# Kernel optimization log

Hardware: AMD Instinct MI355X
Metric: run time of the kernel (lower is better)

Reference implementation:

```python
import jax, jax.numpy as jnp
import numpy as np

B, NV, NC, D, E = 16, 8192, 4096, 128, 49152


def _gru_cell(x, h, w_ih, w_hh, b_ih, b_hh):
    """torch.nn.GRUCell math; gate order r, z, n; weights are (3D, D)."""
    gi = x @ w_ih.T + b_ih
    gh = h @ w_hh.T + b_hh
    ir, iz, inn = jnp.split(gi, 3, axis=-1)
    hr, hz, hn = jnp.split(gh, 3, axis=-1)
    r = jax.nn.sigmoid(ir + hr)
    z = jax.nn.sigmoid(iz + hz)
    n = jnp.tanh(inn + r * hn)
    return (1.0 - z) * n + z * h


def _msg_net(x, w1, b1, w2, b2):
    # Linear -> exact GELU -> Linear (torch nn.GELU default is erf-based)
    return jax.nn.gelu(x @ w1.T + b1, approximate=False) @ w2.T + b2


def _spmm(feats, src_idx, dst_idx, n_out):
    """Binary sparse-matrix @ dense: gather rows at src_idx, segment-sum to dst_idx.
    feats: (B, N_src, D) -> (B, n_out, D). Equivalent to torch.sparse.mm(H, feats[i])."""
    gathered = feats[:, src_idx, :]  # (B, E, D)
    return jax.vmap(lambda g: jax.ops.segment_sum(g, dst_idx, num_segments=n_out))(gathered)


def setup_inputs() -> dict:
    key = jax.random.key(0)
    ks = jax.random.split(key, 20)
    s = 0.05
    inp = {
        "v_feats": jax.random.normal(ks[0], (B, NV, D), jnp.float32),
        "c_feats": jax.random.normal(ks[1], (B, NC, D), jnp.float32),
        "edge_chk": jax.random.randint(ks[2], (E,), 0, NC, jnp.int32),
        "edge_var": jax.random.randint(ks[3], (E,), 0, NV, jnp.int32),
        # msg_net: Linear(D,D) -> GELU -> Linear(D,D)
        "msg_w1": jax.random.normal(ks[4], (D, D), jnp.float32) * s,
        "msg_b1": jnp.zeros((D,), jnp.float32),
        "msg_w2": jax.random.normal(ks[5], (D, D), jnp.float32) * s,
        "msg_b2": jnp.zeros((D,), jnp.float32),
        # var_update GRUCell(D, D)
        "var_w_ih": jax.random.normal(ks[6], (3 * D, D), jnp.float32) * s,
        "var_w_hh": jax.random.normal(ks[7], (3 * D, D), jnp.float32) * s,
        "var_b_ih": jnp.zeros((3 * D,), jnp.float32),
        "var_b_hh": jnp.zeros((3 * D,), jnp.float32),
        # chk_update GRUCell(D, D)
        "chk_w_ih": jax.random.normal(ks[8], (3 * D, D), jnp.float32) * s,
        "chk_w_hh": jax.random.normal(ks[9], (3 * D, D), jnp.float32) * s,
        "chk_b_ih": jnp.zeros((3 * D,), jnp.float32),
        "chk_b_hh": jnp.zeros((3 * D,), jnp.float32),
    }
    return inp


def reference(v_feats, c_feats, edge_chk, edge_var,
              msg_w1, msg_b1, msg_w2, msg_b2,
              var_w_ih, var_w_hh, var_b_ih, var_b_hh,
              chk_w_ih, chk_w_hh, chk_b_ih, chk_b_hh):
    b, nv, d = v_feats.shape
    nc = c_feats.shape[1]
    # variable -> check: H @ v_feats (H is binary, rows=checks, cols=vars)
    v_to_c = _spmm(v_feats, edge_var, edge_chk, nc)        # (B, NC, D)
    v_to_c = _msg_net(v_to_c, msg_w1, msg_b1, msg_w2, msg_b2)
    c_new = _gru_cell(v_to_c.reshape(-1, d), c_feats.reshape(-1, d),
                      chk_w_ih, chk_w_hh, chk_b_ih, chk_b_hh).reshape(b, nc, d)
    # check -> variable: H^T @ c_new
    c_to_v = _spmm(c_new, edge_chk, edge_var, nv)          # (B, NV, D)
    c_to_v = _msg_net(c_to_v, msg_w1, msg_b1, msg_w2, msg_b2)
    v_new = _gru_cell(c_to_v.reshape(-1, d), v_feats.reshape(-1, d),
                      var_w_ih, var_w_hh, var_b_ih, var_b_hh).reshape(b, nv, d)
    return (v_new, c_new)
```

## Files before the change

### kernel.cpp

```cpp
#include <hip/hip_runtime.h>

using u16 = unsigned short;
using u32 = unsigned int;
using u64 = unsigned long long;
typedef short short8 __attribute__((ext_vector_type(8)));
typedef unsigned short ushort8 __attribute__((ext_vector_type(8)));
typedef float f32x4 __attribute__((ext_vector_type(4)));

#define GB  16
#define GNV 8192
#define GNC 4096
#define GD  128
#define GE  49152

#define MFMA __builtin_amdgcn_mfma_f32_16x16x32_bf16
#define SB0() __builtin_amdgcn_sched_barrier(0)


__device__ __forceinline__ u16 f2bf(float f){
    u32 u = __builtin_bit_cast(u32, f);
    u32 r = (u >> 16) & 1u;
    u += 0x7fffu + r;
    return (u16)(u >> 16);
}

__device__ __forceinline__ float bf2f(u16 x){
    return __builtin_bit_cast(float, (u32)x << 16);
}

__device__ __forceinline__ u32 cvtpk(float lo, float hi){
    u32 r;
    asm("v_cvt_pk_bf16_f32 %0, %1, %2" : "=v"(r) : "v"(lo), "v"(hi));
    return r;
}

__device__ __forceinline__ u64 pack4(float a, float b, float c, float d){
    return (u64)cvtpk(a, b) | ((u64)cvtpk(c, d) << 32);
}

__device__ __forceinline__ float sigmoidf_(float x){
    return __fdividef(1.f, 1.f + __expf(-x));
}

__device__ __forceinline__ float tanhf_fast(float x){
    float xc = fminf(15.f, fmaxf(-15.f, x));
    float t  = __expf(2.f * xc);
    return __fdividef(t - 1.f, t + 1.f);
}

__device__ __forceinline__ size_t fidx(int r, int c){
    return ((size_t)(r >> 4) << 11) + ((c >> 5) << 9)
         + (((r & 15) + (((c & 31) >> 3) << 4)) << 3) + (c & 7);
}

__device__ __forceinline__ char* swzp(const void* base, int row, int bc){
    return (char*)base + row * 256 + (bc ^ ((row & 7) << 4));
}

__device__ __forceinline__ short8 ldfrag(const u16* tile, int row, int lane, int ks){
    int bc = ks * 64 + ((lane >> 4) << 4);
    return *(const short8*)swzp(tile, row, bc);
}


__global__ void k_hist(const int* __restrict__ ec, const int* __restrict__ ev,
                       int* cc, int* cv){
    int e = blockIdx.x * 256 + threadIdx.x;
    if (e < GE){ atomicAdd(&cc[ec[e]], 1); atomicAdd(&cv[ev[e]], 1); }
}

__global__ __launch_bounds__(1024) void k_scan2(const int* __restrict__ cnt_c, int* off_c, int* cur_c,
                                                const int* __restrict__ cnt_v, int* off_v, int* cur_v){
    const int* cnt = blockIdx.x ? cnt_v : cnt_c;
    int* off = blockIdx.x ? off_v : off_c;
    int* cur = blockIdx.x ? cur_v : cur_c;
    const int n = blockIdx.x ? GNV : GNC;
    __shared__ int part[1024];
    int tid = threadIdx.x;
    int chunk = n >> 10;
    int base = tid * chunk;
    int s = 0;
    for (int i = 0; i < chunk; ++i) s += cnt[base + i];
    part[tid] = s;
    __syncthreads();
    #pragma unroll
    for (int ofs = 1; ofs < 1024; ofs <<= 1){
        int v = (tid >= ofs) ? part[tid - ofs] : 0;
        __syncthreads();
        part[tid] += v;
        __syncthreads();
    }
    if (tid == 1023) off[n] = part[1023];
    int run = part[tid] - s;
    for (int i = 0; i < chunk; ++i){
        off[base + i] = run; cur[base + i] = run; run += cnt[base + i];
    }
}

__global__ void k_fill(const int* __restrict__ ec, const int* __restrict__ ev,
                       int* cur_c, int* lst_c, int* cur_v, int* lst_v){
    int e = blockIdx.x * 256 + threadIdx.x;
    if (e < GE){
        int c = ec[e], v = ev[e];
        lst_c[atomicAdd(&cur_c[c], 1)] = v;
        lst_v[atomicAdd(&cur_v[v], 1)] = c;
    }
}

__global__ void k_sort2(const int* __restrict__ off_c, int* lst_c,
                        const int* __restrict__ off_v, int* lst_v){
    int i = blockIdx.x * 256 + threadIdx.x;
    const int* off; int* lst; int idx;
    if (i < GNC){ off = off_c; lst = lst_c; idx = i; }
    else if (i < GNC + GNV){ off = off_v; lst = lst_v; idx = i - GNC; }
    else return;
    int s = off[idx], e = off[idx + 1];
    for (int a = s + 1; a < e; ++a){
        int v = lst[a]; int b = a - 1;
        while (b >= s && lst[b] > v){ lst[b + 1] = lst[b]; --b; }
        lst[b + 1] = v;
    }
}

__global__ void k_cvt6(const float* __restrict__ s0, const float* __restrict__ s1,
                       const float* __restrict__ s2, const float* __restrict__ s3,
                       const float* __restrict__ s4, const float* __restrict__ s5,
                       u16* __restrict__ dst){
    int i = blockIdx.x * 256 + threadIdx.x;
    const float* s; int off;
    if (i < 16384)       { s = s0; off = i; }
    else if (i < 32768)  { s = s1; off = i - 16384; }
    else if (i < 81920)  { s = s2; off = i - 32768; }
    else if (i < 131072) { s = s3; off = i - 81920; }
    else if (i < 180224) { s = s4; off = i - 131072; }
    else                 { s = s5; off = i - 180224; }
    dst[i] = f2bf(s[off]);
}


__global__ __launch_bounds__(256) void k_tr2(const float* __restrict__ vfe,
                                             const float* __restrict__ cfe,
                                             u16* __restrict__ vT, u16* __restrict__ vF,
                                             u16* __restrict__ cF){
    const int t = threadIdx.x;
    const int b = t >> 4, d0 = (t & 15) * 8;
    int node = blockIdx.x;
    const float* src; u16* dstT; u16* dstF; int n;
    if (node < GNV){ src = vfe; dstT = vT; dstF = vF; n = GNV; }
    else { node -= GNV; src = cfe; dstT = nullptr; dstF = cF; n = GNC; }
    const float4* s = (const float4*)(src + ((size_t)b * n + node) * GD + d0);
    float4 v0 = s[0], v1 = s[1];
    u64 lo = pack4(v0.x, v0.y, v0.z, v0.w);
    u64 hi = pack4(v1.x, v1.y, v1.z, v1.w);
    if (dstT){
        u64* p = (u64*)(dstT + (size_t)node * 2048 + t * 8);
        p[0] = lo; p[1] = hi;
    }
    u64* q = (u64*)(dstF + fidx(b * n + node, d0));
    q[0] = lo; q[1] = hi;
}


__global__ __launch_bounds__(256) void k_spmm(const u16* __restrict__ srcT,
                                              const int* __restrict__ off,
                                              const int* __restrict__ lst,
                                              u16* __restrict__ dstF, int ndst){
    const int node = blockIdx.x, t = threadIdx.x;
    const int b = t >> 4, d0 = (t & 15) * 8;
    float acc[8];
    #pragma unroll
    for (int i = 0; i < 8; ++i) acc[i] = 0.f;
    const int s = off[node], e = off[node + 1];
    const u16* base = srcT + t * 8;
    for (int a = s; a < e; ++a){
        ushort8 v = *(const ushort8*)(base + (size_t)lst[a] * 2048);
        #pragma unroll
        for (int i = 0; i < 8; ++i) acc[i] += bf2f(v[i]);
    }
    u64* p = (u64*)(dstF + fidx(b * ndst + node, d0));
    p[0] = pack4(acc[0], acc[1], acc[2], acc[3]);
    p[1] = pack4(acc[4], acc[5], acc[6], acc[7]);
}


__global__ __launch_bounds__(512) void k_msg(u16* __restrict__ X,
                                             const u16* __restrict__ W1, const float* __restrict__ b1,
                                             const u16* __restrict__ W2, const float* __restrict__ b2,
                                             int ngroups){
    __shared__ __align__(16) u16 Gs[2][16 * 128];
    const int tid = threadIdx.x, lane = tid & 63, w = tid >> 6;
    const int l15 = lane & 15, rg = lane >> 4;
    const int j = w * 16 + l15;

    short8 w1f[4], w2f[4];
    #pragma unroll
    for (int ks = 0; ks < 4; ++ks){
        w1f[ks] = *(const short8*)(W1 + (size_t)j * 128 + ks * 32 + rg * 8);
        w2f[ks] = *(const short8*)(W2 + (size_t)j * 128 + ks * 32 + rg * 8);
    }
    const float bb1 = b1[j], bb2 = b2[j];

    const int stride = gridDim.x;
    const int ng = ngroups / stride;

    short8 xA[4], xB[4];
    auto loadx = [&](short8* xf, int g){
        const u16* xb = X + ((size_t)g << 11);
        #pragma unroll
        for (int ks = 0; ks < 4; ++ks) xf[ks] = *(const short8*)(xb + ks * 512 + lane * 8);
    };
    auto g1 = [&](const short8* xf, int buf){
        f32x4 acc = {0, 0, 0, 0};
        #pragma unroll
        for (int ks = 0; ks < 4; ++ks) acc = MFMA(xf[ks], w1f[ks], acc, 0, 0, 0);
        #pragma unroll
        for (int i = 0; i < 4; ++i){
            float v = acc[i] + bb1;
            float g = 0.5f * v * (1.f + erff(v * 0.70710678f));
            *(u16*)swzp(Gs[buf], rg * 4 + i, j * 2) = f2bf(g);
        }
    };
    auto g2 = [&](int buf, int g){
        f32x4 acc = {0, 0, 0, 0};
        #pragma unroll
        for (int ks = 0; ks < 4; ++ks)
            acc = MFMA(ldfrag(Gs[buf], l15, lane, ks), w2f[ks], acc, 0, 0, 0);
        #pragma unroll
        for (int i = 0; i < 4; ++i)
            X[fidx(g * 16 + rg * 4 + i, j)] = f2bf(acc[i] + bb2);
    };

    int g = blockIdx.x;
    loadx(xA, g);
    g1(xA, 0);
    for (int k = 0; k < ng; k += 2){
        loadx(xB, g + stride);
        __syncthreads();
        g2(0, g);
        g1(xB, 1);
        if (k + 2 < ng) loadx(xA, g + 2 * stride);
        __syncthreads();
        g2(1, g + stride);
        if (k + 2 < ng) g1(xA, 0);
        g += 2 * stride;
    }
}


__global__ __launch_bounds__(512) void k_gru(const u16* __restrict__ XF, const u16* __restrict__ HF,
                                             const u16* __restrict__ Wih, const float* __restrict__ bih,
                                             const u16* __restrict__ Whh, const float* __restrict__ bhh,
                                             float* __restrict__ Out, u16* __restrict__ OutT,
                                             int logN, int ngroups){
    const int tid = threadIdx.x, lane = tid & 63, w = tid >> 6;
    const int l15 = lane & 15, rg = lane >> 4;
    const int j = w * 16 + l15;
    const int nmask = (1 << logN) - 1;

    short8 wf[6][4];
    #pragma unroll
    for (int g = 0; g < 3; ++g){
        #pragma unroll
        for (int ks = 0; ks < 4; ++ks){
            wf[g][ks]     = *(const short8*)(Wih + (size_t)(g * 128 + j) * 128 + ks * 32 + rg * 8);
            wf[g + 3][ks] = *(const short8*)(Whh + (size_t)(g * 128 + j) * 128 + ks * 32 + rg * 8);
        }
    }
    const float bir = bih[j]       + bhh[j];
    const float biz = bih[128 + j] + bhh[128 + j];
    const float bin = bih[256 + j];
    const float bhn = bhh[256 + j];

    const int h0off = ((j >> 5) << 9) + (((j & 31) >> 3) << 7) + ((rg * 4) << 3) + (j & 7);

    const int stride = gridDim.x;
    const int ng = ngroups / stride;

    short8 xfA[4], hfA[4], xfB[4], hfB[4];
    float h0A[4], h0B[4];

    auto load = [&](short8* xf, short8* hf, float* h0, int g){
        const u16* xb = XF + ((size_t)g << 11);
        const u16* hb = HF + ((size_t)g << 11);
        #pragma unroll
        for (int ks = 0; ks < 4; ++ks){
            xf[ks] = *(const short8*)(xb + ks * 512 + lane * 8);
            hf[ks] = *(const short8*)(hb + ks * 512 + lane * 8);
        }
        #pragma unroll
        for (int i = 0; i < 4; ++i) h0[i] = bf2f(hb[h0off + i * 8]);
    };

    auto comp = [&](const short8* xf, const short8* hf, const float* h0, int g){
        f32x4 ar = {0,0,0,0}, az = {0,0,0,0}, an = {0,0,0,0}, hn = {0,0,0,0};
        #pragma unroll
        for (int ks = 0; ks < 4; ++ks){
            ar = MFMA(xf[ks], wf[0][ks], ar, 0, 0, 0);
            az = MFMA(xf[ks], wf[1][ks], az, 0, 0, 0);
            an = MFMA(xf[ks], wf[2][ks], an, 0, 0, 0);
            ar = MFMA(hf[ks], wf[3][ks], ar, 0, 0, 0);
            az = MFMA(hf[ks], wf[4][ks], az, 0, 0, 0);
            hn = MFMA(hf[ks], wf[5][ks], hn, 0, 0, 0);
        }
        #pragma unroll
        for (int i = 0; i < 4; ++i){
            int r = g * 16 + rg * 4 + i;
            float rr = sigmoidf_(ar[i] + bir);
            float zz = sigmoidf_(az[i] + biz);
            float nn = tanhf_fast(an[i] + bin + rr * (hn[i] + bhn));
            float val = (1.f - zz) * nn + zz * h0[i];
            Out[(size_t)r * GD + j] = val;
            if (OutT){
                int bidx = r >> logN, node = r & nmask;
                OutT[(((size_t)node << 4) + bidx) * GD + j] = f2bf(val);
            }
        }
    };

    int g = blockIdx.x;
    load(xfA, hfA, h0A, g);
    for (int k = 0; k < ng; k += 2){
        load(xfB, hfB, h0B, g + stride);
        SB0();
        comp(xfA, hfA, h0A, g);
        if (k + 2 < ng) load(xfA, hfA, h0A, g + 2 * stride);
        SB0();
        comp(xfB, hfB, h0B, g + stride);
        g += 2 * stride;
    }
}


extern "C" void kernel_launch(void* const* d_in, const int* in_sizes, int n_in,
                              void* d_out, int out_size, void* d_ws, size_t ws_size,
                              hipStream_t stream){
    const float* v_feats  = (const float*)d_in[0];
    const float* c_feats  = (const float*)d_in[1];
    const int*   edge_chk = (const int*)d_in[2];
    const int*   edge_var = (const int*)d_in[3];
    const float* msg_w1   = (const float*)d_in[4];
    const float* msg_b1   = (const float*)d_in[5];
    const float* msg_w2   = (const float*)d_in[6];
    const float* msg_b2   = (const float*)d_in[7];
    const float* var_w_ih = (const float*)d_in[8];
    const float* var_w_hh = (const float*)d_in[9];
    const float* var_b_ih = (const float*)d_in[10];
    const float* var_b_hh = (const float*)d_in[11];
    const float* chk_w_ih = (const float*)d_in[12];
    const float* chk_w_hh = (const float*)d_in[13];
    const float* chk_b_ih = (const float*)d_in[14];
    const float* chk_b_hh = (const float*)d_in[15];

    float* out_v = (float*)d_out;
    float* out_c = out_v + (size_t)GB * GNV * GD;

    char* p = (char*)d_ws;
    auto take = [&](size_t bytes) -> void* {
        void* r = (void*)p; p += (bytes + 255) & ~(size_t)255; return r;
    };
    int* cnt_c = (int*)take(GNC * 4);
    int* cnt_v = (int*)take(GNV * 4);
    int* off_c = (int*)take((GNC + 1) * 4);
    int* off_v = (int*)take((GNV + 1) * 4);
    int* cur_c = (int*)take(GNC * 4);
    int* cur_v = (int*)take(GNV * 4);
    int* lst_c = (int*)take(GE * 4);
    int* lst_v = (int*)take(GE * 4);
    u16* w1b  = (u16*)take((size_t)GD * GD * 2);
    u16* w2b  = (u16*)take((size_t)GD * GD * 2);
    u16* cihb = (u16*)take((size_t)3 * GD * GD * 2);
    u16* chhb = (u16*)take((size_t)3 * GD * GD * 2);
    u16* vihb = (u16*)take((size_t)3 * GD * GD * 2);
    u16* vhhb = (u16*)take((size_t)3 * GD * GD * 2);
    u16* mc = (u16*)take((size_t)GB * GNC * GD * 2);
    u16* mv = (u16*)take((size_t)GB * GNV * GD * 2);
    u16* vT = (u16*)take((size_t)GNV * GB * GD * 2);
    u16* cT = (u16*)take((size_t)GNC * GB * GD * 2);
    u16* vF = (u16*)take((size_t)GB * GNV * GD * 2);
    u16* cF = (u16*)take((size_t)GB * GNC * GD * 2);

    hipMemsetAsync(cnt_c, 0, (GNC + GNV) * 4, stream);
    k_hist<<<(GE + 255) / 256, 256, 0, stream>>>(edge_chk, edge_var, cnt_c, cnt_v);
    k_scan2<<<2, 1024, 0, stream>>>(cnt_c, off_c, cur_c, cnt_v, off_v, cur_v);
    k_fill<<<(GE + 255) / 256, 256, 0, stream>>>(edge_chk, edge_var, cur_c, lst_c, cur_v, lst_v);
    k_sort2<<<(GNC + GNV + 255) / 256, 256, 0, stream>>>(off_c, lst_c, off_v, lst_v);
    k_cvt6<<<896, 256, 0, stream>>>(msg_w1, msg_w2, chk_w_ih, chk_w_hh, var_w_ih, var_w_hh, w1b);
    k_tr2<<<GNV + GNC, 256, 0, stream>>>(v_feats, c_feats, vT, vF, cF);

    k_spmm<<<GNC, 256, 0, stream>>>(vT, off_c, lst_c, mc, GNC);
    k_msg<<<512, 512, 0, stream>>>(mc, w1b, msg_b1, w2b, msg_b2, (GB * GNC) / 16);
    k_gru<<<1024, 512, 0, stream>>>(mc, cF, cihb, chk_b_ih, chhb, chk_b_hh,
                                    out_c, cT, 12, (GB * GNC) / 16);
    k_spmm<<<GNV, 256, 0, stream>>>(cT, off_v, lst_v, mv, GNV);
    k_msg<<<512, 512, 0, stream>>>(mv, w1b, msg_b1, w2b, msg_b2, (GB * GNV) / 16);
    k_gru<<<1024, 512, 0, stream>>>(mv, vF, vihb, var_b_ih, vhhb, var_b_hh,
                                    out_v, (u16*)nullptr, 13, (GB * GNV) / 16);
}
```

Measured before the change: 405.8 us.

## Drop transposed check buffer, gather fp32 GRU output directly, unroll SpMM gathers

The first GRU no longer writes a scattered bf16 node-major copy of its output. The second SpMM instead gathers rows straight from the fp32 output in its batch-major layout, which removes a strided scatter write but doubles the bytes read per gathered row. Both SpMM kernels now unroll by four with independent accumulators so more loads are in flight. The transpose/convert kernel is reorganised to write the fragment layout contiguously per 16-row group.

```diff
diff --git a/kernel.cpp b/kernel.cpp
--- a/kernel.cpp
+++ b/kernel.cpp
@@ -32,6 +32,13 @@
     u32 r;
     asm("v_cvt_pk_bf16_f32 %0, %1, %2" : "=v"(r) : "v"(lo), "v"(hi));
     return r;
+}
+
+__device__ __forceinline__ ushort8 pack8(float4 v0, float4 v1){
+    union { u32 u[4]; ushort8 v; } q;
+    q.u[0] = cvtpk(v0.x, v0.y); q.u[1] = cvtpk(v0.z, v0.w);
+    q.u[2] = cvtpk(v1.x, v1.y); q.u[3] = cvtpk(v1.z, v1.w);
+    return q.v;
 }
 
 __device__ __forceinline__ u64 pack4(float a, float b, float c, float d){
@@ -138,26 +145,25 @@
 }
 
 
-__global__ __launch_bounds__(256) void k_tr2(const float* __restrict__ vfe,
+__global__ __launch_bounds__(256) void k_trg(const float* __restrict__ vfe,
                                              const float* __restrict__ cfe,
                                              u16* __restrict__ vT, u16* __restrict__ vF,
                                              u16* __restrict__ cF){
     const int t = threadIdx.x;
-    const int b = t >> 4, d0 = (t & 15) * 8;
-    int node = blockIdx.x;
-    const float* src; u16* dstT; u16* dstF; int n;
-    if (node < GNV){ src = vfe; dstT = vT; dstF = vF; n = GNV; }
-    else { node -= GNV; src = cfe; dstT = nullptr; dstF = cF; n = GNC; }
-    const float4* s = (const float4*)(src + ((size_t)b * n + node) * GD + d0);
+    const int ks = t >> 6, sub = (t >> 4) & 3, row = t & 15;
+    const int c = ks * 32 + sub * 8;
+    int gg = blockIdx.x;
+    const float* src; u16* dstF; int n, b, node0, grp; u16* dstT = nullptr;
+    if (gg < 8192){ b = gg >> 9; node0 = (gg & 511) << 4; grp = gg;
+                    src = vfe; dstF = vF; n = GNV; dstT = vT; }
+    else { int idx = gg - 8192; b = idx >> 8; node0 = (idx & 255) << 4; grp = idx;
+           src = cfe; dstF = cF; n = GNC; }
+    const float4* s = (const float4*)(src + ((size_t)b * n + node0 + row) * GD + c);
     float4 v0 = s[0], v1 = s[1];
-    u64 lo = pack4(v0.x, v0.y, v0.z, v0.w);
-    u64 hi = pack4(v1.x, v1.y, v1.z, v1.w);
-    if (dstT){
-        u64* p = (u64*)(dstT + (size_t)node * 2048 + t * 8);
-        p[0] = lo; p[1] = hi;
-    }
-    u64* q = (u64*)(dstF + fidx(b * n + node, d0));
-    q[0] = lo; q[1] = hi;
+    ushort8 pk = pack8(v0, v1);
+    *(ushort8*)(dstF + ((size_t)grp << 11) + t * 8) = pk;
+    if (dstT)
+        *(ushort8*)(dstT + ((size_t)(node0 + row) << 11) + b * 128 + c) = pk;
 }
 
 
@@ -167,16 +173,75 @@
                                               u16* __restrict__ dstF, int ndst){
     const int node = blockIdx.x, t = threadIdx.x;
     const int b = t >> 4, d0 = (t & 15) * 8;
-    float acc[8];
-    #pragma unroll
-    for (int i = 0; i < 8; ++i) acc[i] = 0.f;
+    float a0[8], a1[8], a2[8], a3[8];
+    #pragma unroll
+    for (int i = 0; i < 8; ++i){ a0[i] = 0.f; a1[i] = 0.f; a2[i] = 0.f; a3[i] = 0.f; }
     const int s = off[node], e = off[node + 1];
     const u16* base = srcT + t * 8;
-    for (int a = s; a < e; ++a){
-        ushort8 v = *(const ushort8*)(base + (size_t)lst[a] * 2048);
-        #pragma unroll
-        for (int i = 0; i < 8; ++i) acc[i] += bf2f(v[i]);
-    }
+    int a = s;
+    for (; a + 4 <= e; a += 4){
+        ushort8 v0 = *(const ushort8*)(base + ((size_t)lst[a    ] << 11));
+        ushort8 v1 = *(const ushort8*)(base + ((size_t)lst[a + 1] << 11));
+        ushort8 v2 = *(const ushort8*)(base + ((size_t)lst[a + 2] << 11));
+        ushort8 v3 = *(const ushort8*)(base + ((size_t)lst[a + 3] << 11));
+        #pragma unroll
+        for (int i = 0; i < 8; ++i){
+            a0[i] += bf2f(v0[i]); a1[i] += bf2f(v1[i]);
+            a2[i] += bf2f(v2[i]); a3[i] += bf2f(v3[i]);
+        }
+    }
+    for (; a < e; ++a){
+        ushort8 v = *(const ushort8*)(base + ((size_t)lst[a] << 11));
+        #pragma unroll
+        for (int i = 0; i < 8; ++i) a0[i] += bf2f(v[i]);
+    }
+    float acc[8];
+    #pragma unroll
+    for (int i = 0; i < 8; ++i) acc[i] = (a0[i] + a1[i]) + (a2[i] + a3[i]);
+    u64* p = (u64*)(dstF + fidx(b * ndst + node, d0));
+    p[0] = pack4(acc[0], acc[1], acc[2], acc[3]);
+    p[1] = pack4(acc[4], acc[5], acc[6], acc[7]);
+}
+
+
+__global__ __launch_bounds__(256) void k_spmm_f32(const float* __restrict__ src,
+                                                  const int* __restrict__ off,
+                                                  const int* __restrict__ lst,
+                                                  u16* __restrict__ dstF,
+                                                  int ndst, int nsrc){
+    const int node = blockIdx.x, t = threadIdx.x;
+    const int b = t >> 4, d0 = (t & 15) * 8;
+    float a0[8], a1[8], a2[8], a3[8];
+    #pragma unroll
+    for (int i = 0; i < 8; ++i){ a0[i] = 0.f; a1[i] = 0.f; a2[i] = 0.f; a3[i] = 0.f; }
+    const int s = off[node], e = off[node + 1];
+    const float* base = src + (size_t)b * nsrc * GD + d0;
+    int a = s;
+    for (; a + 4 <= e; a += 4){
+        const float4* p0 = (const float4*)(base + ((size_t)lst[a    ] << 7));
+        const float4* p1 = (const float4*)(base + ((size_t)lst[a + 1] << 7));
+        const float4* p2 = (const float4*)(base + ((size_t)lst[a + 2] << 7));
+        const float4* p3 = (const float4*)(base + ((size_t)lst[a + 3] << 7));
+        float4 x0 = p0[0], y0 = p0[1], x1 = p1[0], y1 = p1[1];
+        float4 x2 = p2[0], y2 = p2[1], x3 = p3[0], y3 = p3[1];
+        a0[0]+=x0.x; a0[1]+=x0.y; a0[2]+=x0.z; a0[3]+=x0.w;
+        a0[4]+=y0.x; a0[5]+=y0.y; a0[6]+=y0.z; a0[7]+=y0.w;
+        a1[0]+=x1.x; a1[1]+=x1.y; a1[2]+=x1.z; a1[3]+=x1.w;
+        a1[4]+=y1.x; a1[5]+=y1.y; a1[6]+=y1.z; a1[7]+=y1.w;
+        a2[0]+=x2.x; a2[1]+=x2.y; a2[2]+=x2.z; a2[3]+=x2.w;
+        a2[4]+=y2.x; a2[5]+=y2.y; a2[6]+=y2.z; a2[7]+=y2.w;
+        a3[0]+=x3.x; a3[1]+=x3.y; a3[2]+=x3.z; a3[3]+=x3.w;
+        a3[4]+=y3.x; a3[5]+=y3.y; a3[6]+=y3.z; a3[7]+=y3.w;
+    }
+    for (; a < e; ++a){
+        const float4* p = (const float4*)(base + ((size_t)lst[a] << 7));
+        float4 x = p[0], y = p[1];
+        a0[0]+=x.x; a0[1]+=x.y; a0[2]+=x.z; a0[3]+=x.w;
+        a0[4]+=y.x; a0[5]+=y.y; a0[6]+=y.z; a0[7]+=y.w;
+    }
+    float acc[8];
+    #pragma unroll
+    for (int i = 0; i < 8; ++i) acc[i] = (a0[i] + a1[i]) + (a2[i] + a3[i]);
     u64* p = (u64*)(dstF + fidx(b * ndst + node, d0));
     p[0] = pack4(acc[0], acc[1], acc[2], acc[3]);
     p[1] = pack4(acc[4], acc[5], acc[6], acc[7]);
@@ -250,12 +315,10 @@
 __global__ __launch_bounds__(512) void k_gru(const u16* __restrict__ XF, const u16* __restrict__ HF,
                                              const u16* __restrict__ Wih, const float* __restrict__ bih,
                                              const u16* __restrict__ Whh, const float* __restrict__ bhh,
-                                             float* __restrict__ Out, u16* __restrict__ OutT,
-                                             int logN, int ngroups){
+                                             float* __restrict__ Out, int ngroups){
     const int tid = threadIdx.x, lane = tid & 63, w = tid >> 6;
     const int l15 = lane & 15, rg = lane >> 4;
     const int j = w * 16 + l15;
-    const int nmask = (1 << logN) - 1;
 
     short8 wf[6][4];
     #pragma unroll
@@ -308,12 +371,7 @@
             float rr = sigmoidf_(ar[i] + bir);
             float zz = sigmoidf_(az[i] + biz);
             float nn = tanhf_fast(an[i] + bin + rr * (hn[i] + bhn));
-            float val = (1.f - zz) * nn + zz * h0[i];
-            Out[(size_t)r * GD + j] = val;
-            if (OutT){
-                int bidx = r >> logN, node = r & nmask;
-                OutT[(((size_t)node << 4) + bidx) * GD + j] = f2bf(val);
-            }
+            Out[(size_t)r * GD + j] = (1.f - zz) * nn + zz * h0[i];
         }
     };
 
@@ -375,7 +433,6 @@
     u16* mc = (u16*)take((size_t)GB * GNC * GD * 2);
     u16* mv = (u16*)take((size_t)GB * GNV * GD * 2);
     u16* vT = (u16*)take((size_t)GNV * GB * GD * 2);
-    u16* cT = (u16*)take((size_t)GNC * GB * GD * 2);
     u16* vF = (u16*)take((size_t)GB * GNV * GD * 2);
     u16* cF = (u16*)take((size_t)GB * GNC * GD * 2);
 
@@ -385,14 +442,14 @@
     k_fill<<<(GE + 255) / 256, 256, 0, stream>>>(edge_chk, edge_var, cur_c, lst_c, cur_v, lst_v);
     k_sort2<<<(GNC + GNV + 255) / 256, 256, 0, stream>>>(off_c, lst_c, off_v, lst_v);
     k_cvt6<<<896, 256, 0, stream>>>(msg_w1, msg_w2, chk_w_ih, chk_w_hh, var_w_ih, var_w_hh, w1b);
-    k_tr2<<<GNV + GNC, 256, 0, stream>>>(v_feats, c_feats, vT, vF, cF);
+    k_trg<<<8192 + 4096, 256, 0, stream>>>(v_feats, c_feats, vT, vF, cF);
 
     k_spmm<<<GNC, 256, 0, stream>>>(vT, off_c, lst_c, mc, GNC);
     k_msg<<<512, 512, 0, stream>>>(mc, w1b, msg_b1, w2b, msg_b2, (GB * GNC) / 16);
     k_gru<<<1024, 512, 0, stream>>>(mc, cF, cihb, chk_b_ih, chhb, chk_b_hh,
-                                    out_c, cT, 12, (GB * GNC) / 16);
-    k_spmm<<<GNV, 256, 0, stream>>>(cT, off_v, lst_v, mv, GNV);
+                                    out_c, (GB * GNC) / 16);
+    k_spmm_f32<<<GNV, 256, 0, stream>>>(out_c, off_v, lst_v, mv, GNV, GNC);
     k_msg<<<512, 512, 0, stream>>>(mv, w1b, msg_b1, w2b, msg_b2, (GB * GNV) / 16);
     k_gru<<<1024, 512, 0, stream>>>(mv, vF, vihb, var_b_ih, vhhb, var_b_hh,
-                                    out_v, (u16*)nullptr, 13, (GB * GNV) / 16);
-}
+                                    out_v, (GB * GNV) / 16);
+}
```

Result: faster. 389.3 us (-4.1%).

## Fuse spmm, message MLP and GRU into one kernel per direction

Applied to the files above, without the earlier changes.

Replaces the separate spmm, msg-net and GRU kernels with a single persistent kernel per direction. Each block gathers and sums a 16-node tile, then runs both MLP layers and the GRU in shared memory, keeping intermediates out of global memory. The hidden state is read from a node-major transposed bf16 copy instead of a separate fragment-layout copy, and the transposed output is staged through LDS for coalesced writes. The cost is several __syncthreads per tile, higher register pressure from holding all weight fragments, and no overlap of the gather latency with the MFMA work.

```diff
diff --git a/kernel.cpp b/kernel.cpp
--- a/kernel.cpp
+++ b/kernel.cpp
@@ -14,7 +14,6 @@
 #define GE  49152
 
 #define MFMA __builtin_amdgcn_mfma_f32_16x16x32_bf16
-#define SB0() __builtin_amdgcn_sched_barrier(0)
 
 
 __device__ __forceinline__ u16 f2bf(float f){
@@ -34,6 +33,13 @@
     return r;
 }
 
+__device__ __forceinline__ ushort8 pack8(float4 v0, float4 v1){
+    union { u32 u[4]; ushort8 v; } q;
+    q.u[0] = cvtpk(v0.x, v0.y); q.u[1] = cvtpk(v0.z, v0.w);
+    q.u[2] = cvtpk(v1.x, v1.y); q.u[3] = cvtpk(v1.z, v1.w);
+    return q.v;
+}
+
 __device__ __forceinline__ u64 pack4(float a, float b, float c, float d){
     return (u64)cvtpk(a, b) | ((u64)cvtpk(c, d) << 32);
 }
@@ -46,11 +52,6 @@
     float xc = fminf(15.f, fmaxf(-15.f, x));
     float t  = __expf(2.f * xc);
     return __fdividef(t - 1.f, t + 1.f);
-}
-
-__device__ __forceinline__ size_t fidx(int r, int c){
-    return ((size_t)(r >> 4) << 11) + ((c >> 5) << 9)
-         + (((r & 15) + (((c & 31) >> 3) << 4)) << 3) + (c & 7);
 }
 
 __device__ __forceinline__ char* swzp(const void* base, int row, int bc){
@@ -138,126 +139,45 @@
 }
 
 
-__global__ __launch_bounds__(256) void k_tr2(const float* __restrict__ vfe,
+__global__ __launch_bounds__(256) void k_trn(const float* __restrict__ vfe,
                                              const float* __restrict__ cfe,
-                                             u16* __restrict__ vT, u16* __restrict__ vF,
-                                             u16* __restrict__ cF){
+                                             u16* __restrict__ vT, u16* __restrict__ cfT){
     const int t = threadIdx.x;
     const int b = t >> 4, d0 = (t & 15) * 8;
     int node = blockIdx.x;
-    const float* src; u16* dstT; u16* dstF; int n;
-    if (node < GNV){ src = vfe; dstT = vT; dstF = vF; n = GNV; }
-    else { node -= GNV; src = cfe; dstT = nullptr; dstF = cF; n = GNC; }
+    const float* src; u16* dst; int n;
+    if (node < GNV){ src = vfe; dst = vT; n = GNV; }
+    else { node -= GNV; src = cfe; dst = cfT; n = GNC; }
     const float4* s = (const float4*)(src + ((size_t)b * n + node) * GD + d0);
-    float4 v0 = s[0], v1 = s[1];
-    u64 lo = pack4(v0.x, v0.y, v0.z, v0.w);
-    u64 hi = pack4(v1.x, v1.y, v1.z, v1.w);
-    if (dstT){
-        u64* p = (u64*)(dstT + (size_t)node * 2048 + t * 8);
-        p[0] = lo; p[1] = hi;
-    }
-    u64* q = (u64*)(dstF + fidx(b * n + node, d0));
-    q[0] = lo; q[1] = hi;
-}
-
-
-__global__ __launch_bounds__(256) void k_spmm(const u16* __restrict__ srcT,
-                                              const int* __restrict__ off,
-                                              const int* __restrict__ lst,
-                                              u16* __restrict__ dstF, int ndst){
-    const int node = blockIdx.x, t = threadIdx.x;
-    const int b = t >> 4, d0 = (t & 15) * 8;
-    float acc[8];
-    #pragma unroll
-    for (int i = 0; i < 8; ++i) acc[i] = 0.f;
-    const int s = off[node], e = off[node + 1];
-    const u16* base = srcT + t * 8;
-    for (int a = s; a < e; ++a){
-        ushort8 v = *(const ushort8*)(base + (size_t)lst[a] * 2048);
-        #pragma unroll
-        for (int i = 0; i < 8; ++i) acc[i] += bf2f(v[i]);
-    }
-    u64* p = (u64*)(dstF + fidx(b * ndst + node, d0));
-    p[0] = pack4(acc[0], acc[1], acc[2], acc[3]);
-    p[1] = pack4(acc[4], acc[5], acc[6], acc[7]);
-}
-
-
-__global__ __launch_bounds__(512) void k_msg(u16* __restrict__ X,
-                                             const u16* __restrict__ W1, const float* __restrict__ b1,
-                                             const u16* __restrict__ W2, const float* __restrict__ b2,
-                                             int ngroups){
-    __shared__ __align__(16) u16 Gs[2][16 * 128];
+    *(ushort8*)(dst + ((size_t)node << 11) + b * 128 + d0) = pack8(s[0], s[1]);
+}
+
+
+__global__ __launch_bounds__(512) void k_fused(
+    const u16* __restrict__ srcT, const int* __restrict__ off, const int* __restrict__ lst,
+    const u16* __restrict__ HT,
+    const u16* __restrict__ W1, const float* __restrict__ b1,
+    const u16* __restrict__ W2, const float* __restrict__ b2,
+    const u16* __restrict__ Wih, const float* __restrict__ bih,
+    const u16* __restrict__ Whh, const float* __restrict__ bhh,
+    float* __restrict__ Out, u16* __restrict__ OutT,
+    int logN, int ngroups)
+{
+    __shared__ __align__(16) u16 Xs[16 * 128];
+    __shared__ __align__(16) u16 Hs[16 * 128];
+    __shared__ __align__(16) u16 Gs[16 * 128];
+    __shared__ __align__(16) u16 Ms[16 * 128];
+    __shared__ __align__(16) u16 Os[16 * 128];
     const int tid = threadIdx.x, lane = tid & 63, w = tid >> 6;
     const int l15 = lane & 15, rg = lane >> 4;
     const int j = w * 16 + l15;
 
-    short8 w1f[4], w2f[4];
+    short8 w1f[4], w2f[4], wf[6][4];
     #pragma unroll
     for (int ks = 0; ks < 4; ++ks){
         w1f[ks] = *(const short8*)(W1 + (size_t)j * 128 + ks * 32 + rg * 8);
         w2f[ks] = *(const short8*)(W2 + (size_t)j * 128 + ks * 32 + rg * 8);
     }
-    const float bb1 = b1[j], bb2 = b2[j];
-
-    const int stride = gridDim.x;
-    const int ng = ngroups / stride;
-
-    short8 xA[4], xB[4];
-    auto loadx = [&](short8* xf, int g){
-        const u16* xb = X + ((size_t)g << 11);
-        #pragma unroll
-        for (int ks = 0; ks < 4; ++ks) xf[ks] = *(const short8*)(xb + ks * 512 + lane * 8);
-    };
-    auto g1 = [&](const short8* xf, int buf){
-        f32x4 acc = {0, 0, 0, 0};
-        #pragma unroll
-        for (int ks = 0; ks < 4; ++ks) acc = MFMA(xf[ks], w1f[ks], acc, 0, 0, 0);
-        #pragma unroll
-        for (int i = 0; i < 4; ++i){
-            float v = acc[i] + bb1;
-            float g = 0.5f * v * (1.f + erff(v * 0.70710678f));
-            *(u16*)swzp(Gs[buf], rg * 4 + i, j * 2) = f2bf(g);
-        }
-    };
-    auto g2 = [&](int buf, int g){
-        f32x4 acc = {0, 0, 0, 0};
-        #pragma unroll
-        for (int ks = 0; ks < 4; ++ks)
-            acc = MFMA(ldfrag(Gs[buf], l15, lane, ks), w2f[ks], acc, 0, 0, 0);
-        #pragma unroll
-        for (int i = 0; i < 4; ++i)
-            X[fidx(g * 16 + rg * 4 + i, j)] = f2bf(acc[i] + bb2);
-    };
-
-    int g = blockIdx.x;
-    loadx(xA, g);
-    g1(xA, 0);
-    for (int k = 0; k < ng; k += 2){
-        loadx(xB, g + stride);
-        __syncthreads();
-        g2(0, g);
-        g1(xB, 1);
-        if (k + 2 < ng) loadx(xA, g + 2 * stride);
-        __syncthreads();
-        g2(1, g + stride);
-        if (k + 2 < ng) g1(xA, 0);
-        g += 2 * stride;
-    }
-}
-
-
-__global__ __launch_bounds__(512) void k_gru(const u16* __restrict__ XF, const u16* __restrict__ HF,
-                                             const u16* __restrict__ Wih, const float* __restrict__ bih,
-                                             const u16* __restrict__ Whh, const float* __restrict__ bhh,
-                                             float* __restrict__ Out, u16* __restrict__ OutT,
-                                             int logN, int ngroups){
-    const int tid = threadIdx.x, lane = tid & 63, w = tid >> 6;
-    const int l15 = lane & 15, rg = lane >> 4;
-    const int j = w * 16 + l15;
-    const int nmask = (1 << logN) - 1;
-
-    short8 wf[6][4];
     #pragma unroll
     for (int g = 0; g < 3; ++g){
         #pragma unroll
@@ -266,67 +186,105 @@
             wf[g + 3][ks] = *(const short8*)(Whh + (size_t)(g * 128 + j) * 128 + ks * 32 + rg * 8);
         }
     }
+    const float bb1 = b1[j], bb2 = b2[j];
     const float bir = bih[j]       + bhh[j];
     const float biz = bih[128 + j] + bhh[128 + j];
     const float bin = bih[256 + j];
     const float bhn = bhh[256 + j];
 
-    const int h0off = ((j >> 5) << 9) + (((j & 31) >> 3) << 7) + ((rg * 4) << 3) + (j & 7);
-
-    const int stride = gridDim.x;
-    const int ng = ngroups / stride;
-
-    short8 xfA[4], hfA[4], xfB[4], hfB[4];
-    float h0A[4], h0B[4];
-
-    auto load = [&](short8* xf, short8* hf, float* h0, int g){
-        const u16* xb = XF + ((size_t)g << 11);
-        const u16* hb = HF + ((size_t)g << 11);
-        #pragma unroll
-        for (int ks = 0; ks < 4; ++ks){
-            xf[ks] = *(const short8*)(xb + ks * 512 + lane * 8);
-            hf[ks] = *(const short8*)(hb + ks * 512 + lane * 8);
-        }
-        #pragma unroll
-        for (int i = 0; i < 4; ++i) h0[i] = bf2f(hb[h0off + i * 8]);
-    };
-
-    auto comp = [&](const short8* xf, const short8* hf, const float* h0, int g){
-        f32x4 ar = {0,0,0,0}, az = {0,0,0,0}, an = {0,0,0,0}, hn = {0,0,0,0};
-        #pragma unroll
-        for (int ks = 0; ks < 4; ++ks){
-            ar = MFMA(xf[ks], wf[0][ks], ar, 0, 0, 0);
-            az = MFMA(xf[ks], wf[1][ks], az, 0, 0, 0);
-            an = MFMA(xf[ks], wf[2][ks], an, 0, 0, 0);
-            ar = MFMA(hf[ks], wf[3][ks], ar, 0, 0, 0);
-            az = MFMA(hf[ks], wf[4][ks], az, 0, 0, 0);
-            hn = MFMA(hf[ks], wf[5][ks], hn, 0, 0, 0);
-        }
-        #pragma unroll
-        for (int i = 0; i < 4; ++i){
-            int r = g * 16 + rg * 4 + i;
-            float rr = sigmoidf_(ar[i] + bir);
-            float zz = sigmoidf_(az[i] + biz);
-            float nn = tanhf_fast(an[i] + bin + rr * (hn[i] + bhn));
-            float val = (1.f - zz) * nn + zz * h0[i];
-            Out[(size_t)r * GD + j] = val;
-            if (OutT){
-                int bidx = r >> logN, node = r & nmask;
-                OutT[(((size_t)node << 4) + bidx) * GD + j] = f2bf(val);
-            }
-        }
-    };
-
-    int g = blockIdx.x;
-    load(xfA, hfA, h0A, g);
-    for (int k = 0; k < ng; k += 2){
-        load(xfB, hfB, h0B, g + stride);
-        SB0();
-        comp(xfA, hfA, h0A, g);
-        if (k + 2 < ng) load(xfA, hfA, h0A, g + 2 * stride);
-        SB0();
-        comp(xfB, hfB, h0B, g + stride);
-        g += 2 * stride;
+    const int grow = tid >> 5;
+    const int q    = tid & 31;
+    const int d0   = q * 4;
+    const int gpb_shift = logN - 4;
+
+    for (int g = blockIdx.x; g < ngroups; g += gridDim.x){
+        const int b = g >> gpb_shift;
+        const int node0 = (g & ((1 << gpb_shift) - 1)) << 4;
+        const int mynode = node0 + grow;
+
+        {
+            u64 hv = *(const u64*)(HT + (((size_t)mynode) << 11) + b * 128 + d0);
+            *(u64*)swzp(Hs, grow, q * 8) = hv;
+
+            const int s = off[mynode], e = off[mynode + 1];
+            const u16* base = srcT + b * 128 + d0;
+            float a0[4] = {0,0,0,0}, a1[4] = {0,0,0,0};
+            int a = s;
+            for (; a + 2 <= e; a += 2){
+                u64 v0 = *(const u64*)(base + ((size_t)lst[a]     << 11));
+                u64 v1 = *(const u64*)(base + ((size_t)lst[a + 1] << 11));
+                #pragma unroll
+                for (int i = 0; i < 4; ++i){
+                    a0[i] += bf2f((u16)(v0 >> (16 * i)));
+                    a1[i] += bf2f((u16)(v1 >> (16 * i)));
+                }
+            }
+            if (a < e){
+                u64 v0 = *(const u64*)(base + ((size_t)lst[a] << 11));
+                #pragma unroll
+                for (int i = 0; i < 4; ++i) a0[i] += bf2f((u16)(v0 >> (16 * i)));
+            }
+            *(u64*)swzp(Xs, grow, q * 8) =
+                pack4(a0[0] + a1[0], a0[1] + a1[1], a0[2] + a1[2], a0[3] + a1[3]);
+        }
+        __syncthreads();
+
+        {
+            f32x4 acc = {0, 0, 0, 0};
+            #pragma unroll
+            for (int ks = 0; ks < 4; ++ks)
+                acc = MFMA(ldfrag(Xs, l15, lane, ks), w1f[ks], acc, 0, 0, 0);
+            #pragma unroll
+            for (int i = 0; i < 4; ++i){
+                float v = acc[i] + bb1;
+                float ge = 0.5f * v * (1.f + erff(v * 0.70710678f));
+                *(u16*)swzp(Gs, rg * 4 + i, j * 2) = f2bf(ge);
+            }
+        }
+        __syncthreads();
+
+        {
+            f32x4 acc = {0, 0, 0, 0};
+            #pragma unroll
+            for (int ks = 0; ks < 4; ++ks)
+                acc = MFMA(ldfrag(Gs, l15, lane, ks), w2f[ks], acc, 0, 0, 0);
+            #pragma unroll
+            for (int i = 0; i < 4; ++i)
+                *(u16*)swzp(Ms, rg * 4 + i, j * 2) = f2bf(acc[i] + bb2);
+        }
+        __syncthreads();
+
+        {
+            f32x4 ar = {0,0,0,0}, az = {0,0,0,0}, an = {0,0,0,0}, hn = {0,0,0,0};
+            #pragma unroll
+            for (int ks = 0; ks < 4; ++ks){
+                short8 x = ldfrag(Ms, l15, lane, ks);
+                short8 h = ldfrag(Hs, l15, lane, ks);
+                ar = MFMA(x, wf[0][ks], ar, 0, 0, 0);
+                az = MFMA(x, wf[1][ks], az, 0, 0, 0);
+                an = MFMA(x, wf[2][ks], an, 0, 0, 0);
+                ar = MFMA(h, wf[3][ks], ar, 0, 0, 0);
+                az = MFMA(h, wf[4][ks], az, 0, 0, 0);
+                hn = MFMA(h, wf[5][ks], hn, 0, 0, 0);
+            }
+            #pragma unroll
+            for (int i = 0; i < 4; ++i){
+                int rl = rg * 4 + i;
+                float h0 = bf2f(*(const u16*)swzp(Hs, rl, j * 2));
+                float rr = sigmoidf_(ar[i] + bir);
+                float zz = sigmoidf_(az[i] + biz);
+                float nn = tanhf_fast(an[i] + bin + rr * (hn[i] + bhn));
+                float val = (1.f - zz) * nn + zz * h0;
+                Out[((size_t)g * 16 + rl) * GD + j] = val;
+                if (OutT) *(u16*)swzp(Os, rl, j * 2) = f2bf(val);
+            }
+        }
+        if (OutT){
+            __syncthreads();
+            u64 ov = *(const u64*)swzp(Os, grow, q * 8);
+            *(u64*)(OutT + (((size_t)mynode) << 11) + b * 128 + d0) = ov;
+        }
+        __syncthreads();
     }
 }
 
@@ -372,12 +330,9 @@
     u16* chhb = (u16*)take((size_t)3 * GD * GD * 2);
     u16* vihb = (u16*)take((size_t)3 * GD * GD * 2);
     u16* vhhb = (u16*)take((size_t)3 * GD * GD * 2);
-    u16* mc = (u16*)take((size_t)GB * GNC * GD * 2);
-    u16* mv = (u16*)take((size_t)GB * GNV * GD * 2);
-    u16* vT = (u16*)take((size_t)GNV * GB * GD * 2);
-    u16* cT = (u16*)take((size_t)GNC * GB * GD * 2);
-    u16* vF = (u16*)take((size_t)GB * GNV * GD * 2);
-    u16* cF = (u16*)take((size_t)GB * GNC * GD * 2);
+    u16* vT  = (u16*)take((size_t)GNV * GB * GD * 2);
+    u16* cfT = (u16*)take((size_t)GNC * GB * GD * 2);
+    u16* cT  = (u16*)take((size_t)GNC * GB * GD * 2);
 
     hipMemsetAsync(cnt_c, 0, (GNC + GNV) * 4, stream);
     k_hist<<<(GE + 255) / 256, 256, 0, stream>>>(edge_chk, edge_var, cnt_c, cnt_v);
@@ -385,14 +340,14 @@
     k_fill<<<(GE + 255) / 256, 256, 0, stream>>>(edge_chk, edge_var, cur_c, lst_c, cur_v, lst_v);
     k_sort2<<<(GNC + GNV + 255) / 256, 256, 0, stream>>>(off_c, lst_c, off_v, lst_v);
     k_cvt6<<<896, 256, 0, stream>>>(msg_w1, msg_w2, chk_w_ih, chk_w_hh, var_w_ih, var_w_hh, w1b);
-    k_tr2<<<GNV + GNC, 256, 0, stream>>>(v_feats, c_feats, vT, vF, cF);
-
-    k_spmm<<<GNC, 256, 0, stream>>>(vT, off_c, lst_c, mc, GNC);
-    k_msg<<<512, 512, 0, stream>>>(mc, w1b, msg_b1, w2b, msg_b2, (GB * GNC) / 16);
-    k_gru<<<1024, 512, 0, stream>>>(mc, cF, cihb, chk_b_ih, chhb, chk_b_hh,
-                                    out_c, cT, 12, (GB * GNC) / 16);
-    k_spmm<<<GNV, 256, 0, stream>>>(cT, off_v, lst_v, mv, GNV);
-    k_msg<<<512, 512, 0, stream>>>(mv, w1b, msg_b1, w2b, msg_b2, (GB * GNV) / 16);
-    k_gru<<<1024, 512, 0, stream>>>(mv, vF, vihb, var_b_ih, vhhb, var_b_hh,
-                                    out_v, (u16*)nullptr, 13, (GB * GNV) / 16);
-}
+    k_trn<<<GNV + GNC, 256, 0, stream>>>(v_feats, c_feats, vT, cfT);
+
+    k_fused<<<2048, 512, 0, stream>>>(vT, off_c, lst_c, cfT,
+                                      w1b, msg_b1, w2b, msg_b2,
+                                      cihb, chk_b_ih, chhb, chk_b_hh,
+                                      out_c, cT, 12, (GB * GNC) / 16);
+    k_fused<<<2048, 512, 0, stream>>>(cT, off_v, lst_v, vT,
+                                      w1b, msg_b1, w2b, msg_b2,
+                                      vihb, var_b_ih, vhhb, var_b_hh,
+                                      out_v, (u16*)nullptr, 13, (GB * GNV) / 16);
+}
```

Result: slower. 548.1 us (+35.1%).
